# Kernel tuning notes

Measured on AMD Instinct MI355X. Metric: run time of the kernel, lower is better.

Reference implementation:

```python
import jax, jax.numpy as jnp
import numpy as np

B, IDIM, ODIM, MSIZE = 8192, 4096, 4096, 128
ICOUNT = (IDIM + MSIZE - 1) // MSIZE        # 32
MCOUNT = (max(IDIM, ODIM) + MSIZE - 1) // MSIZE  # 32
OCOUNT = (ODIM + MSIZE - 1) // MSIZE        # 32


def setup_inputs() -> dict:
    key = jax.random.key(0)
    ks = jax.random.split(key, 7)
    s_in = 1.0 / np.sqrt(ICOUNT)
    s_m = 1.0 / np.sqrt(MSIZE)
    s_out = 1.0 / np.sqrt(MCOUNT)
    return {
        "x": jax.random.normal(ks[0], (B, IDIM), dtype=jnp.float32),
        "W_in": jax.random.normal(ks[1], (MCOUNT, ICOUNT), dtype=jnp.float32) * s_in,
        "b_in": jax.random.normal(ks[2], (MCOUNT,), dtype=jnp.float32) * s_in,
        "W_mods": jax.random.normal(ks[3], (MCOUNT, MSIZE, MSIZE), dtype=jnp.float32) * s_m,
        "b_mods": jax.random.normal(ks[4], (MCOUNT, MSIZE), dtype=jnp.float32) * s_m,
        "W_out": jax.random.normal(ks[5], (OCOUNT, MCOUNT), dtype=jnp.float32) * s_out,
        "b_out": jax.random.normal(ks[6], (OCOUNT,), dtype=jnp.float32) * s_out,
        "odim": ODIM,
    }


def reference(x, W_in, b_in, W_mods, b_mods, W_out, b_out, odim):
    msize = W_mods.shape[-1]
    b = x.shape[0]
    idim = x.shape[-1]
    rem = idim % msize  # static
    if rem != 0:
        x = jnp.pad(x, ((0, 0), (0, msize - rem)))
    icount = x.shape[-1] // msize
    # reshape to blocks then tail_permute (swap last two axes)
    x = x.reshape(b, icount, msize).swapaxes(-1, -2)      # [B, msize, icount]
    x = jnp.einsum('bmi,ci->bmc', x, W_in) + b_in          # fcin -> [B, msize, mcount]
    x = x.swapaxes(-1, -2)                                 # [B, mcount, msize]
    # per-block submodule: Linear(msize->msize) per block, vectorized over blocks
    x = jnp.einsum('bcm,cnm->bcn', x, W_mods) + b_mods     # [B, mcount, msize]
    x = x.swapaxes(-1, -2)                                 # [B, msize, mcount]
    x = jnp.einsum('bmc,oc->bmo', x, W_out) + b_out        # fcout -> [B, msize, ocount]
    x = x.reshape(b, -1)[:, :odim]                         # [B, odim]
    return x  # act = Identity
```

## Files before the change

kernel.cpp:

```cpp
#include <hip/hip_runtime.h>
#include <stdint.h>


#define BT    8
#define NTHR  512
#define GRID  1024
#define IDIM  4096
#define ODIM  4096

typedef __attribute__((ext_vector_type(8))) __bf16 bf16x8;
typedef __attribute__((ext_vector_type(4))) float  floatx4;

union BF8 { uint32_t w[4]; unsigned short h[8]; bf16x8 v; };

__device__ __forceinline__ unsigned short f2bf(float f) {
    uint32_t u = __builtin_bit_cast(uint32_t, f);
    u += 0x7fffu + ((u >> 16) & 1u);
    return (unsigned short)(u >> 16);
}

#define YROW 132
__device__ __forceinline__ int yaddr(int c, int bt, int m) {
    return (c * 8 + bt) * YROW + ((((m >> 2) ^ (c & 7))) << 2) + (m & 3);
}
#define WROW 36

template<bool WBF16>
__global__ __launch_bounds__(NTHR, 4)
void tinymod_fused(const float* __restrict__ x,
                   const float* __restrict__ W_in,
                   const float* __restrict__ b_in,
                   const void*  __restrict__ wmods,
                   const float* __restrict__ b_mods,
                   const float* __restrict__ W_out,
                   const float* __restrict__ b_out,
                   float* __restrict__ out)
{
    __shared__ unsigned short ylds[256 * YROW]    __attribute__((aligned(16)));
    __shared__ unsigned short wch [16 * 8 * WROW] __attribute__((aligned(16)));

    const int tid  = threadIdx.x;
    const int lane = tid & 63;
    const int wave = tid >> 6;
    const int l15  = lane & 15;
    const int grp  = lane >> 4;
    const int row0 = blockIdx.x * BT;

    const float bin0 = b_in[l15],  bin1 = b_in[16 + l15];
    const float bo0  = b_out[l15], bo1  = b_out[16 + l15];
    BF8 winf[2], woutf[2];
    #pragma unroll
    for (int cc = 0; cc < 2; cc++) {
        const float* p = W_in  + (l15 + 16*cc) * 32 + grp * 8;
        const float* q = W_out + (l15 + 16*cc) * 32 + grp * 8;
        #pragma unroll
        for (int j = 0; j < 8; j++) { winf[cc].h[j] = f2bf(p[j]); woutf[cc].h[j] = f2bf(q[j]); }
    }

    const float* xb = x + (row0 + wave) * IDIM + l15;
    float xr[8];
    #pragma unroll
    for (int j = 0; j < 8; j++) xr[j] = xb[(grp*8 + j) * 128];

    for (int mb = 0; mb < 8; mb++) {
        float xn[8];
        if (mb < 7) {
            #pragma unroll
            for (int j = 0; j < 8; j++) xn[j] = xb[(grp*8 + j) * 128 + (mb + 1) * 16];
        }
        BF8 a;
        #pragma unroll
        for (int j = 0; j < 8; j++) a.h[j] = f2bf(xr[j]);
        #pragma unroll
        for (int cc = 0; cc < 2; cc++) {
            floatx4 acc = {0.f, 0.f, 0.f, 0.f};
            acc = __builtin_amdgcn_mfma_f32_16x16x32_bf16(a.v, winf[cc].v, acc, 0, 0, 0);
            const float bi = cc ? bin1 : bin0;
            unsigned short h[4];
            #pragma unroll
            for (int r = 0; r < 4; r++) h[r] = f2bf(acc[r] + bi);
            uint2 pk;
            pk.x = (uint32_t)h[0] | ((uint32_t)h[1] << 16);
            pk.y = (uint32_t)h[2] | ((uint32_t)h[3] << 16);
            *(uint2*)&ylds[yaddr(l15 + 16*cc, wave, mb*16 + grp*4)] = pk;
        }
        if (mb < 7) {
            #pragma unroll
            for (int j = 0; j < 8; j++) xr[j] = xn[j];
        }
    }
    __syncthreads();

    const unsigned short* __restrict__ wm16 = (const unsigned short*)wmods;
    const float*          __restrict__ wm32 = (const float*)wmods;
    const int btA = l15 & 7;

    for (int nb = 0; nb < 8; nb++) {
        floatx4 acc[4];
        float   bm[4];
        #pragma unroll
        for (int ci = 0; ci < 4; ci++) {
            const int c = 4*wave + ci;
            bm[ci] = b_mods[c*128 + nb*16 + l15];
            floatx4 s = {0.f, 0.f, 0.f, 0.f};
            #pragma unroll
            for (int kc = 0; kc < 4; kc++) {
                const int m0 = kc*32 + grp*8;
                BF8 a2;
                const uint2 u0 = *(const uint2*)&ylds[yaddr(c, btA, m0)];
                const uint2 u1 = *(const uint2*)&ylds[yaddr(c, btA, m0 + 4)];
                a2.w[0] = u0.x; a2.w[1] = u0.y; a2.w[2] = u1.x; a2.w[3] = u1.y;
                BF8 b;
                const int wbase = (c*128 + nb*16 + l15)*128 + kc*32 + grp*8;
                if (WBF16) {
                    const uint4 bv = *(const uint4*)&wm16[wbase];
                    b.w[0] = bv.x; b.w[1] = bv.y; b.w[2] = bv.z; b.w[3] = bv.w;
                } else {
                    const float* wp = wm32 + wbase;
                    #pragma unroll
                    for (int j = 0; j < 8; j++) b.h[j] = f2bf(wp[j]);
                }
                s = __builtin_amdgcn_mfma_f32_16x16x32_bf16(a2.v, b.v, s, 0, 0, 0);
            }
            acc[ci] = s;
        }
        if (grp < 2) {
            #pragma unroll
            for (int r = 0; r < 4; r++) {
                const int bt = grp*4 + r;
                unsigned short h[4];
                #pragma unroll
                for (int ci = 0; ci < 4; ci++) h[ci] = f2bf(acc[ci][r] + bm[ci]);
                uint2 pk;
                pk.x = (uint32_t)h[0] | ((uint32_t)h[1] << 16);
                pk.y = (uint32_t)h[2] | ((uint32_t)h[3] << 16);
                *(uint2*)&wch[(l15*8 + bt)*WROW + 4*wave] = pk;
            }
        }
        __syncthreads();

        const int np = 2*wave + (l15 >> 3);
        BF8 a3;
        {
            const int off = (np*8 + btA)*WROW + grp*8;
            const uint2 u0 = *(const uint2*)&wch[off];
            const uint2 u1 = *(const uint2*)&wch[off + 4];
            a3.w[0] = u0.x; a3.w[1] = u0.y; a3.w[2] = u1.x; a3.w[3] = u1.y;
        }
        __syncthreads();

        #pragma unroll
        for (int oc = 0; oc < 2; oc++) {
            floatx4 v = {0.f, 0.f, 0.f, 0.f};
            v = __builtin_amdgcn_mfma_f32_16x16x32_bf16(a3.v, woutf[oc].v, v, 0, 0, 0);
            const float bo = oc ? bo1 : bo0;
            #pragma unroll
            for (int r = 0; r < 4; r++) {
                const int R   = grp*4 + r;
                const int nlo = R >> 3;
                const int bt  = R & 7;
                out[(row0 + bt)*ODIM + (nb*16 + 2*wave + nlo)*32 + oc*16 + l15] = v[r] + bo;
            }
        }
    }
}

__global__ void wmods_to_bf16(const float* __restrict__ w, unsigned short* __restrict__ o) {
    const int i = (blockIdx.x * 256 + threadIdx.x) * 4;
    const float4 f = *(const float4*)(w + i);
    uint2 pk;
    pk.x = (uint32_t)f2bf(f.x) | ((uint32_t)f2bf(f.y) << 16);
    pk.y = (uint32_t)f2bf(f.z) | ((uint32_t)f2bf(f.w) << 16);
    *(uint2*)(o + i) = pk;
}

extern "C" void kernel_launch(void* const* d_in, const int* in_sizes, int n_in,
                              void* d_out, int out_size, void* d_ws, size_t ws_size,
                              hipStream_t stream)
{
    const float* x     = (const float*)d_in[0];
    const float* W_in  = (const float*)d_in[1];
    const float* b_in  = (const float*)d_in[2];
    const float* Wm    = (const float*)d_in[3];
    const float* b_m   = (const float*)d_in[4];
    const float* W_out = (const float*)d_in[5];
    const float* b_out = (const float*)d_in[6];
    float* out = (float*)d_out;

    const size_t wm_elems = 32u * 128u * 128u;
    if (ws_size >= wm_elems * sizeof(unsigned short)) {
        unsigned short* wbf = (unsigned short*)d_ws;
        wmods_to_bf16<<<(int)(wm_elems / (256 * 4)), 256, 0, stream>>>(Wm, wbf);
        tinymod_fused<true><<<GRID, NTHR, 0, stream>>>(x, W_in, b_in, (const void*)wbf,
                                                       b_m, W_out, b_out, out);
    } else {
        tinymod_fused<false><<<GRID, NTHR, 0, stream>>>(x, W_in, b_in, (const void*)Wm,
                                                        b_m, W_out, b_out, out);
    }
}
```

Baseline: 354.4 us.

## Process 16 rows per block with 1024 threads and register-resident module activations

Doubles the batch tile to 16 rows per block with 16 waves, so each wave handles 2 modules instead of 4. The MFMA M dimension is now fully used by batch rows, where half the lanes were previously wasted. Module-stage A fragments are loaded from LDS once into registers and reused across all 8 output chunks, and the LDS layouts are changed to padded row strides in place of the XOR swizzle. W_mods traffic is also amortized over twice as many rows. In exchange, LDS use per block roughly doubles and 1024-thread blocks under launch_bounds(…,4) may limit occupancy or cause register pressure.

```diff
diff --git a/kernel.cpp b/kernel.cpp
--- a/kernel.cpp
+++ b/kernel.cpp
@@ -2,9 +2,9 @@
 #include <stdint.h>
 
 
-#define BT    8
-#define NTHR  512
-#define GRID  1024
+#define BT    16
+#define NTHR  1024
+#define GRID  512
 #define IDIM  4096
 #define ODIM  4096
 
@@ -19,11 +19,10 @@
     return (unsigned short)(u >> 16);
 }
 
-#define YROW 132
-__device__ __forceinline__ int yaddr(int c, int bt, int m) {
-    return (c * 8 + bt) * YROW + ((((m >> 2) ^ (c & 7))) << 2) + (m & 3);
-}
-#define WROW 36
+#define YP_BT 136
+#define YP_C  2184
+#define WP_BT 36
+#define WP_N  584
 
 template<bool WBF16>
 __global__ __launch_bounds__(NTHR, 4)
@@ -36,8 +35,8 @@
                    const float* __restrict__ b_out,
                    float* __restrict__ out)
 {
-    __shared__ unsigned short ylds[256 * YROW]    __attribute__((aligned(16)));
-    __shared__ unsigned short wch [16 * 8 * WROW] __attribute__((aligned(16)));
+    __shared__ unsigned short ylds[32 * YP_C] __attribute__((aligned(16)));
+    __shared__ unsigned short wch [16 * WP_N] __attribute__((aligned(16)));
 
     const int tid  = threadIdx.x;
     const int lane = tid & 63;
@@ -82,7 +81,7 @@
             uint2 pk;
             pk.x = (uint32_t)h[0] | ((uint32_t)h[1] << 16);
             pk.y = (uint32_t)h[2] | ((uint32_t)h[3] << 16);
-            *(uint2*)&ylds[yaddr(l15 + 16*cc, wave, mb*16 + grp*4)] = pk;
+            *(uint2*)&ylds[(l15 + 16*cc)*YP_C + wave*YP_BT + mb*16 + grp*4] = pk;
         }
         if (mb < 7) {
             #pragma unroll
@@ -91,25 +90,31 @@
     }
     __syncthreads();
 
+    BF8 af[2][4];
+    #pragma unroll
+    for (int ci = 0; ci < 2; ci++) {
+        const int c = 2*wave + ci;
+        #pragma unroll
+        for (int kc = 0; kc < 4; kc++) {
+            const uint4 v = *(const uint4*)&ylds[c*YP_C + l15*YP_BT + kc*32 + grp*8];
+            af[ci][kc].w[0] = v.x; af[ci][kc].w[1] = v.y;
+            af[ci][kc].w[2] = v.z; af[ci][kc].w[3] = v.w;
+        }
+    }
+
     const unsigned short* __restrict__ wm16 = (const unsigned short*)wmods;
     const float*          __restrict__ wm32 = (const float*)wmods;
-    const int btA = l15 & 7;
 
     for (int nb = 0; nb < 8; nb++) {
-        floatx4 acc[4];
-        float   bm[4];
+        floatx4 acc[2];
+        float   bm[2];
         #pragma unroll
-        for (int ci = 0; ci < 4; ci++) {
-            const int c = 4*wave + ci;
+        for (int ci = 0; ci < 2; ci++) {
+            const int c = 2*wave + ci;
             bm[ci] = b_mods[c*128 + nb*16 + l15];
             floatx4 s = {0.f, 0.f, 0.f, 0.f};
             #pragma unroll
             for (int kc = 0; kc < 4; kc++) {
-                const int m0 = kc*32 + grp*8;
-                BF8 a2;
-                const uint2 u0 = *(const uint2*)&ylds[yaddr(c, btA, m0)];
-                const uint2 u1 = *(const uint2*)&ylds[yaddr(c, btA, m0 + 4)];
-                a2.w[0] = u0.x; a2.w[1] = u0.y; a2.w[2] = u1.x; a2.w[3] = u1.y;
                 BF8 b;
                 const int wbase = (c*128 + nb*16 + l15)*128 + kc*32 + grp*8;
                 if (WBF16) {
@@ -120,29 +125,22 @@
                     #pragma unroll
                     for (int j = 0; j < 8; j++) b.h[j] = f2bf(wp[j]);
                 }
-                s = __builtin_amdgcn_mfma_f32_16x16x32_bf16(a2.v, b.v, s, 0, 0, 0);
+                s = __builtin_amdgcn_mfma_f32_16x16x32_bf16(af[ci][kc].v, b.v, s, 0, 0, 0);
             }
             acc[ci] = s;
         }
-        if (grp < 2) {
-            #pragma unroll
-            for (int r = 0; r < 4; r++) {
-                const int bt = grp*4 + r;
-                unsigned short h[4];
-                #pragma unroll
-                for (int ci = 0; ci < 4; ci++) h[ci] = f2bf(acc[ci][r] + bm[ci]);
-                uint2 pk;
-                pk.x = (uint32_t)h[0] | ((uint32_t)h[1] << 16);
-                pk.y = (uint32_t)h[2] | ((uint32_t)h[3] << 16);
-                *(uint2*)&wch[(l15*8 + bt)*WROW + 4*wave] = pk;
-            }
+        #pragma unroll
+        for (int r = 0; r < 4; r++) {
+            unsigned short h0 = f2bf(acc[0][r] + bm[0]);
+            unsigned short h1 = f2bf(acc[1][r] + bm[1]);
+            const uint32_t pk = (uint32_t)h0 | ((uint32_t)h1 << 16);
+            *(uint32_t*)&wch[l15*WP_N + (grp*4 + r)*WP_BT + 2*wave] = pk;
         }
         __syncthreads();
 
-        const int np = 2*wave + (l15 >> 3);
         BF8 a3;
         {
-            const int off = (np*8 + btA)*WROW + grp*8;
+            const int off = wave*WP_N + l15*WP_BT + grp*8;
             const uint2 u0 = *(const uint2*)&wch[off];
             const uint2 u1 = *(const uint2*)&wch[off + 4];
             a3.w[0] = u0.x; a3.w[1] = u0.y; a3.w[2] = u1.x; a3.w[3] = u1.y;
@@ -154,12 +152,11 @@
             floatx4 v = {0.f, 0.f, 0.f, 0.f};
             v = __builtin_amdgcn_mfma_f32_16x16x32_bf16(a3.v, woutf[oc].v, v, 0, 0, 0);
             const float bo = oc ? bo1 : bo0;
+            float* po = out + row0*ODIM + (nb*16 + wave)*32 + oc*16 + l15;
             #pragma unroll
             for (int r = 0; r < 4; r++) {
-                const int R   = grp*4 + r;
-                const int nlo = R >> 3;
-                const int bt  = R & 7;
-                out[(row0 + bt)*ODIM + (nb*16 + 2*wave + nlo)*32 + oc*16 + l15] = v[r] + bo;
+                const int bt = grp*4 + r;
+                po[bt*ODIM] = v[r] + bo;
             }
         }
     }
```

After: 306.4 us. 1.16x faster.
